# Optimization experiments

Measured on AMD Instinct MI355X. Metric: run time of the kernel, lower is better.

The kernel has to match this reference:

```python
import jax, jax.numpy as jnp
import numpy as np

LN_EPS = 1e-6  # flax.linen.LayerNorm default
ETA_BASE = 1.0  # TTTLinear default


def _ln(u, g, b):
    mu = u.mean(-1, keepdims=True)
    var = ((u - mu) ** 2).mean(-1, keepdims=True)
    return (u - mu) / jnp.sqrt(var + LN_EPS) * g + b


def setup_inputs() -> dict:
    key = jax.random.key(0)
    ks = jax.random.split(key, 8)
    B, T, D, Bd = 16, 2048, 512, 64
    s_in = 1.0 / np.sqrt(D)
    s_bn = 1.0 / np.sqrt(Bd)
    return {
        "x": jax.random.normal(ks[0], (B, T, D), jnp.float32),
        "Wk": jax.random.normal(ks[1], (D, Bd), jnp.float32) * s_in,
        "bk": jnp.zeros((Bd,), jnp.float32),
        "Wv": jax.random.normal(ks[2], (D, Bd), jnp.float32) * s_in,
        "bv": jnp.zeros((Bd,), jnp.float32),
        "Wq": jax.random.normal(ks[3], (D, Bd), jnp.float32) * s_in,
        "bq": jnp.zeros((Bd,), jnp.float32),
        "Wo": jax.random.normal(ks[4], (Bd, D), jnp.float32) * s_bn,
        "bo": jnp.zeros((D,), jnp.float32),
        "ln_g": jnp.ones((Bd,), jnp.float32),
        "ln_b": jnp.zeros((Bd,), jnp.float32),
        "lr_w": jax.random.normal(ks[5], (D,), jnp.float32) * s_in,
        "lr_b": jnp.zeros((), jnp.float32),
        "W0": jax.random.normal(ks[6], (Bd, Bd), jnp.float32) * 0.01,
    }


def reference(x, Wk, bk, Wv, bv, Wq, bq, Wo, bo, ln_g, ln_b, lr_w, lr_b, W0):
    # Sequential TTT-Linear: per-token SGD update of fast weights W (per batch element).
    B, T, D = x.shape
    Bd = W0.shape[0]

    def ssl_loss(W, k, v):
        # f(k; W) = k + LN(k @ W.T); loss = mean((f - v)^2)
        pred = k + _ln(k @ W.T, ln_g, ln_b)
        return jnp.mean((pred - v) ** 2)

    grad_fn = jax.vmap(jax.value_and_grad(ssl_loss))  # over batch

    def step(W, x_t):
        # x_t: (B, D); W: (B, Bd, Bd)
        k = x_t @ Wk + bk
        v = x_t @ Wv + bv
        loss, gW = grad_fn(W, k, v)
        eta = ETA_BASE * jax.nn.sigmoid(x_t @ lr_w + lr_b)  # (B,)
        W_new = W - eta[:, None, None] * gW
        q = x_t @ Wq + bq
        h = q + _ln(jnp.einsum('bi,boi->bo', q, W_new), ln_g, ln_b)
        z = h @ Wo + bo
        return W_new, (z, loss)

    W_init = jnp.broadcast_to(W0, (B, Bd, Bd))
    W_final, (zs, losses) = jax.lax.scan(step, W_init, jnp.swapaxes(x, 0, 1))
    z = jnp.swapaxes(zs, 0, 1)  # (B, T, D_out)
    return z
```

## Files before the change

### kernel.cpp

```cpp
#include <hip/hip_runtime.h>
#include <math.h>

#define NB 16
#define T  2048
#define D  512
#define BD 64
#define BT (NB*T)

#define OFF_K   0
#define OFF_V   (BT*BD)
#define OFF_Q   (2*BT*BD)
#define OFF_ETA (3*BT*BD)
#define OFF_H   (3*BT*BD + BT)

#define GSTRIDE 544
#define NCHUNK  (BT/16)

#define RL(x, i) __int_as_float(__builtin_amdgcn_readlane(__float_as_int(x), (i)))

__device__ __forceinline__ float wave_allsum(float x) {
  x += __int_as_float(__builtin_amdgcn_update_dpp(
      0, __float_as_int(x), 0x111, 0xf, 0xf, true));
  x += __int_as_float(__builtin_amdgcn_update_dpp(
      0, __float_as_int(x), 0x112, 0xf, 0xf, true));
  x += __int_as_float(__builtin_amdgcn_update_dpp(
      0, __float_as_int(x), 0x114, 0xf, 0xf, true));
  x += __int_as_float(__builtin_amdgcn_update_dpp(
      0, __float_as_int(x), 0x118, 0xf, 0xf, true));
  x += __int_as_float(__builtin_amdgcn_update_dpp(
      0, __float_as_int(x), 0x142, 0xa, 0xf, false));
  x += __int_as_float(__builtin_amdgcn_update_dpp(
      0, __float_as_int(x), 0x143, 0xc, 0xf, false));
  return RL(x, 63);
}

__device__ __forceinline__ void lds_barrier() {
  __builtin_amdgcn_sched_barrier(0);
  __builtin_amdgcn_s_waitcnt(0xC07F);
  __builtin_amdgcn_s_barrier();
  __builtin_amdgcn_sched_barrier(0);
}

__global__ __launch_bounds__(256) void proj_kernel(
    const float* __restrict__ x,
    const float* __restrict__ Wk, const float* __restrict__ bk,
    const float* __restrict__ Wv, const float* __restrict__ bv,
    const float* __restrict__ Wq, const float* __restrict__ bq,
    float* __restrict__ Kout, float* __restrict__ Vout,
    float* __restrict__ Qout) {
  __shared__ __align__(16) float xs[16 * D];
  const int tid = threadIdx.x;
  const size_t row0 = (size_t)blockIdx.x * 16;
  const float4* xg = (const float4*)(x + row0 * D);
  float4* xs4 = (float4*)xs;
#pragma unroll
  for (int i = 0; i < 8; i++) xs4[i * 256 + tid] = xg[i * 256 + tid];
  __syncthreads();
  const int col = tid & 63;
  const int rg = tid >> 6;

  float ak0 = 0.f, ak1 = 0.f, ak2 = 0.f, ak3 = 0.f;
  float av0 = 0.f, av1 = 0.f, av2 = 0.f, av3 = 0.f;
  float aq0 = 0.f, aq1 = 0.f, aq2 = 0.f, aq3 = 0.f;
  for (int d = 0; d < D; d += 4) {
    float wk0 = Wk[(d + 0) * BD + col];
    float wk1 = Wk[(d + 1) * BD + col];
    float wk2 = Wk[(d + 2) * BD + col];
    float wk3 = Wk[(d + 3) * BD + col];
    float wv0 = Wv[(d + 0) * BD + col];
    float wv1 = Wv[(d + 1) * BD + col];
    float wv2 = Wv[(d + 2) * BD + col];
    float wv3 = Wv[(d + 3) * BD + col];
    float wq0 = Wq[(d + 0) * BD + col];
    float wq1 = Wq[(d + 1) * BD + col];
    float wq2 = Wq[(d + 2) * BD + col];
    float wq3 = Wq[(d + 3) * BD + col];
    const float* xb = xs + (rg * 4) * D + d;
    float4 x0 = *(const float4*)(xb);
    float4 x1 = *(const float4*)(xb + D);
    float4 x2 = *(const float4*)(xb + 2 * D);
    float4 x3 = *(const float4*)(xb + 3 * D);
    ak0 += x0.x * wk0 + x0.y * wk1 + x0.z * wk2 + x0.w * wk3;
    ak1 += x1.x * wk0 + x1.y * wk1 + x1.z * wk2 + x1.w * wk3;
    ak2 += x2.x * wk0 + x2.y * wk1 + x2.z * wk2 + x2.w * wk3;
    ak3 += x3.x * wk0 + x3.y * wk1 + x3.z * wk2 + x3.w * wk3;
    av0 += x0.x * wv0 + x0.y * wv1 + x0.z * wv2 + x0.w * wv3;
    av1 += x1.x * wv0 + x1.y * wv1 + x1.z * wv2 + x1.w * wv3;
    av2 += x2.x * wv0 + x2.y * wv1 + x2.z * wv2 + x2.w * wv3;
    av3 += x3.x * wv0 + x3.y * wv1 + x3.z * wv2 + x3.w * wv3;
    aq0 += x0.x * wq0 + x0.y * wq1 + x0.z * wq2 + x0.w * wq3;
    aq1 += x1.x * wq0 + x1.y * wq1 + x1.z * wq2 + x1.w * wq3;
    aq2 += x2.x * wq0 + x2.y * wq1 + x2.z * wq2 + x2.w * wq3;
    aq3 += x3.x * wq0 + x3.y * wq1 + x3.z * wq2 + x3.w * wq3;
  }
  float bbk = bk[col], bbv = bv[col], bbq = bq[col];
  const size_t r0 = row0 + rg * 4;
  Kout[(r0 + 0) * BD + col] = ak0 + bbk;
  Kout[(r0 + 1) * BD + col] = ak1 + bbk;
  Kout[(r0 + 2) * BD + col] = ak2 + bbk;
  Kout[(r0 + 3) * BD + col] = ak3 + bbk;
  Vout[(r0 + 0) * BD + col] = av0 + bbv;
  Vout[(r0 + 1) * BD + col] = av1 + bbv;
  Vout[(r0 + 2) * BD + col] = av2 + bbv;
  Vout[(r0 + 3) * BD + col] = av3 + bbv;
  Qout[(r0 + 0) * BD + col] = aq0 + bbq;
  Qout[(r0 + 1) * BD + col] = aq1 + bbq;
  Qout[(r0 + 2) * BD + col] = aq2 + bbq;
  Qout[(r0 + 3) * BD + col] = aq3 + bbq;
}

__global__ __launch_bounds__(256) void eta_kernel(const float* __restrict__ x,
                                                  const float* __restrict__ lr_w,
                                                  const float* __restrict__ lr_b,
                                                  float* __restrict__ eta) {
  const int tid = threadIdx.x;
  const int lane = tid & 63;
  const int wv = tid >> 6;
  const size_t r = (size_t)blockIdx.x * 4 + wv;
  const float* xr = x + r * D + lane * 8;
  float4 a = *(const float4*)xr;
  float4 b = *(const float4*)(xr + 4);
  const float* lw = lr_w + lane * 8;
  float4 la = *(const float4*)lw;
  float4 lb = *(const float4*)(lw + 4);
  float p = a.x * la.x + a.y * la.y + a.z * la.z + a.w * la.w +
            b.x * lb.x + b.y * lb.y + b.z * lb.z + b.w * lb.w;
#pragma unroll
  for (int m = 32; m > 0; m >>= 1) p += __shfl_xor(p, m, 64);
  if (lane == 0) eta[r] = 1.0f / (1.0f + expf(-(p + lr_b[0])));
}

__global__ __launch_bounds__(256) void gram_kernel(
    const float* __restrict__ K, const float* __restrict__ V,
    const float* __restrict__ Q, const float* __restrict__ ln_g,
    const float* __restrict__ ln_b, float* __restrict__ G) {
  __shared__ __align__(16) float sK[16][64], sQ[16][64], sV[16][64];
  __shared__ float sg[64], sb[64];
  const int tid = threadIdx.x;
  const size_t row0 = (size_t)blockIdx.x * 16;
  ((float4*)sK)[tid] = ((const float4*)(K + row0 * BD))[tid];
  ((float4*)sQ)[tid] = ((const float4*)(Q + row0 * BD))[tid];
  ((float4*)sV)[tid] = ((const float4*)(V + row0 * BD))[tid];
  if (tid < 64) { sg[tid] = ln_g[tid]; sb[tid] = ln_b[tid]; }
  __syncthreads();
  const int i = tid >> 4, t = tid & 15;
  float kk = 0.f, kq = 0.f;
#pragma unroll
  for (int d = 0; d < 64; d += 4) {
    float4 a4 = *(const float4*)&sK[i][d];
    float4 b4 = *(const float4*)&sK[t][d];
    float4 c4 = *(const float4*)&sQ[t][d];
    kk += a4.x * b4.x + a4.y * b4.y + a4.z * b4.z + a4.w * b4.w;
    kq += a4.x * c4.x + a4.y * c4.y + a4.z * c4.z + a4.w * c4.w;
  }
  size_t gb = (size_t)blockIdx.x * GSTRIDE;
  G[gb + i * 16 + t] = kk;
  G[gb + 256 + i * 16 + t] = kq;
  if (tid < 16) {
    float sc = 0.f;
    for (int d = 0; d < 64; d++)
      sc += sg[d] * (sK[tid][d] + sb[d] - sV[tid][d]);
    G[gb + 512 + tid] = sc;
  }
}

__global__ __launch_bounds__(256, 1)
void ttt_seq_kernel(
    const float* __restrict__ Kin, const float* __restrict__ Vin,
    const float* __restrict__ Qin, const float* __restrict__ eta_in,
    const float* __restrict__ W0, const float* __restrict__ ln_g,
    const float* __restrict__ ln_b, float* __restrict__ Hout,
    const float* __restrict__ gram) {
  __shared__ __align__(16) float2 part2[16][4][64];
  __shared__ __align__(16) float kls[16][64];
  __shared__ __align__(16) float qls[16][64];
  const int tid = threadIdx.x;
  const int lane = tid & 63;
  const int wvu = __builtin_amdgcn_readfirstlane(tid) >> 6;
  const int b = blockIdx.x;

  float w[16];
  {
    const float4* w04 = (const float4*)(W0 + (size_t)lane * BD + wvu * 16);
#pragma unroll
    for (int i = 0; i < 4; i++) {
      float4 t4 = w04[i];
      w[4 * i] = t4.x; w[4 * i + 1] = t4.y; w[4 * i + 2] = t4.z; w[4 * i + 3] = t4.w;
    }
  }
  const float g = ln_g[lane];
  const float bet = ln_b[lane];
  const float a = g * g;
  const float A2 = wave_allsum(a);

  size_t base = (size_t)b * T * BD;
  size_t ebase = (size_t)b * T;

  float krow[16], qrow[16], vrow[16];
#pragma unroll
  for (int r = 0; r < 16; r++) {
    krow[r] = Kin[base + r * BD + lane];
    qrow[r] = Qin[base + r * BD + lane];
    vrow[r] = Vin[base + r * BD + lane];
  }
  float ev  = eta_in[ebase + lane];
  float evn = eta_in[ebase + 64 + lane];

  float u2sv[4], qsv[4];

  for (int c64 = 0; c64 < 32; c64++) {
    size_t eoff = (size_t)(c64 + 2) * 64;
    if (eoff >= T) eoff = 0;
    float ev2 = eta_in[ebase + eoff + lane];

    for (int cc = 0; cc < 4; cc++) {
      const size_t gb = (size_t)(b * 128 + c64 * 4 + cc) * GSTRIDE;
      float KKr[15], KQr[16];
#pragma unroll
      for (int t = 0; t < 15; t++) KKr[t] = gram[gb + t * 16 + lane];
#pragma unroll
      for (int t = 0; t < 16; t++) KQr[t] = gram[gb + 256 + t * 16 + lane];
      float SCv = gram[gb + 512 + lane];

#pragma unroll
      for (int r = 0; r < 16; r++) {
        kls[r][lane] = krow[r];
        qls[r][lane] = qrow[r];
      }
      float4 kuf[3][4], quf[3][4];
#pragma unroll
      for (int r = 0; r < 3; r++) {
        const float4* kp = (const float4*)&kls[r][wvu * 16];
        const float4* qp = (const float4*)&qls[r][wvu * 16];
#pragma unroll
        for (int i = 0; i < 4; i++) { kuf[r][i] = kp[i]; quf[r][i] = qp[i]; }
      }
      float u0[16], p0[16];
#pragma unroll
      for (int r = 0; r < 16; r++) {
        const int bf = r % 3;
        float uu0 = 0.f, uu1 = 0.f, uu2 = 0.f, uu3 = 0.f;
        float pp0 = 0.f, pp1 = 0.f, pp2 = 0.f, pp3 = 0.f;
#pragma unroll
        for (int i = 0; i < 4; i++) {
          uu0 += kuf[bf][i].x * w[4 * i + 0];
          uu1 += kuf[bf][i].y * w[4 * i + 1];
          uu2 += kuf[bf][i].z * w[4 * i + 2];
          uu3 += kuf[bf][i].w * w[4 * i + 3];
          pp0 += quf[bf][i].x * w[4 * i + 0];
          pp1 += quf[bf][i].y * w[4 * i + 1];
          pp2 += quf[bf][i].z * w[4 * i + 2];
          pp3 += quf[bf][i].w * w[4 * i + 3];
        }
        part2[r][wvu][lane] = make_float2((uu0 + uu1) + (uu2 + uu3),
                                          (pp0 + pp1) + (pp2 + pp3));
        if (r < 13) {
          const float4* kp = (const float4*)&kls[r + 3][wvu * 16];
          const float4* qp = (const float4*)&qls[r + 3][wvu * 16];
#pragma unroll
          for (int i = 0; i < 4; i++) { kuf[bf][i] = kp[i]; quf[bf][i] = qp[i]; }
        }
      }

      lds_barrier();

#pragma unroll
      for (int r = 0; r < 16; r++) {
        float2 pA = part2[r][0][lane];
        float2 pB = part2[r][1][lane];
        float2 pC = part2[r][2][lane];
        float2 pD = part2[r][3][lane];
        u0[r] = (pA.x + pB.x) + (pC.x + pD.x);
        p0[r] = (pA.y + pB.y) + (pC.y + pD.y);
      }

      float pcorr[4];
#pragma unroll
      for (int fi = 0; fi < 4; fi++) pcorr[fi] = 0.f;

#pragma unroll
      for (int t = 0; t < 16; t++) {
        float u = u0[t];
        float kcur = krow[t], vcur = vrow[t], qcur = qrow[t];
        float ecur = RL(ev, cc * 16 + t);
        float c0 = g * (kcur + bet - vcur);

        float Su   = wave_allsum(u);
        float Suu  = wave_allsum(u * u);
        float Sau  = wave_allsum(a * u);
        float Sauu = wave_allsum(a * u * u);
        float Scu  = wave_allsum(c0 * u);
        float Sc   = RL(SCv, t);

        float mu = Su * (1.0f / 64);
        float var = Suu * (1.0f / 64) - mu * mu;
        float rstd = rsqrtf(var + 1e-6f);
        float xh = (u - mu) * rstd;
        float Axh   = rstd * (Sau - mu * A2);
        float Scxh  = rstd * (Scu - mu * Sc);
        float Saxh2 = rstd * rstd * (Sauu - 2.0f * mu * Sau + mu * mu * A2);
        float s1 = (2.0f / 64) * (Sc + Axh);
        float s2 = (2.0f / 64) * (Scxh + Saxh2);
        float dxh = (2.0f / 64) * (c0 + a * xh);
        float dldu = rstd * (dxh - s1 * (1.0f / 64) - xh * (s2 * (1.0f / 64)));
        float coef = -ecur * dldu;

        if (t < 15)
          u0[t + 1] += coef * RL(KKr[t], t + 1);
#pragma unroll
        for (int s = t + 2; s < 16; s++)
          u0[s] += coef * RL(KKr[t], s);

#pragma unroll
        for (int fi = 0; fi < 4; fi++) {
          if (t <= 4 * fi + 3) {
            const int town = 4 * fi + wvu;
            float term = coef * RL(KQr[t], town);
            if (t <= town) pcorr[fi] += term;
          }
        }

        {
          const float4* kp = (const float4*)&kls[t][wvu * 16];
#pragma unroll
          for (int i = 0; i < 4; i++) {
            float4 k4 = kp[i];
            w[4 * i + 0] += coef * k4.x;
            w[4 * i + 1] += coef * k4.y;
            w[4 * i + 2] += coef * k4.z;
            w[4 * i + 3] += coef * k4.w;
          }
        }

        if ((t & 3) == wvu) { u2sv[t >> 2] = p0[t]; qsv[t >> 2] = qcur; }

        krow[t] = Kin[base + 16 * BD + lane];
        qrow[t] = Qin[base + 16 * BD + lane];
        vrow[t] = Vin[base + 16 * BD + lane];
        base += BD;
      }

#pragma unroll
      for (int fi = 0; fi < 4; fi++) {
        float u2 = u2sv[fi] + pcorr[fi];
        float Su2  = wave_allsum(u2);
        float Suu2 = wave_allsum(u2 * u2);
        float mu2 = Su2 * (1.0f / 64);
        float rstd2 = rsqrtf(Suu2 * (1.0f / 64) - mu2 * mu2 + 1e-6f);
        int tt = 4 * fi + wvu;
        Hout[base - (size_t)(16 - tt) * BD + lane] =
            qsv[fi] + (u2 - mu2) * rstd2 * g + bet;
      }

      lds_barrier();
    }
    ev = evn; evn = ev2;
  }
}

__global__ __launch_bounds__(256) void outproj_kernel(
    const float* __restrict__ H, const float* __restrict__ Wo,
    const float* __restrict__ bo, float* __restrict__ out) {
  __shared__ __align__(16) float ht[16 * BD];
  const int tid = threadIdx.x;
  const size_t row0 = (size_t)blockIdx.x * 16;
  ((float4*)ht)[tid] = ((const float4*)(H + row0 * BD))[tid];
  __syncthreads();
  float acc0[16], acc1[16];
#pragma unroll
  for (int r = 0; r < 16; r++) { acc0[r] = 0.f; acc1[r] = 0.f; }
  for (int kk = 0; kk < BD; kk++) {
    float w0 = Wo[kk * D + tid];
    float w1 = Wo[kk * D + tid + 256];
#pragma unroll
    for (int r = 0; r < 16; r++) {
      float hv = ht[r * BD + kk];
      acc0[r] += hv * w0;
      acc1[r] += hv * w1;
    }
  }
  float b0 = bo[tid], b1 = bo[tid + 256];
#pragma unroll
  for (int r = 0; r < 16; r++) {
    out[(row0 + r) * D + tid] = acc0[r] + b0;
    out[(row0 + r) * D + tid + 256] = acc1[r] + b1;
  }
}

extern "C" void kernel_launch(void* const* d_in, const int* in_sizes, int n_in,
                              void* d_out, int out_size, void* d_ws,
                              size_t ws_size, hipStream_t stream) {
  (void)in_sizes; (void)n_in; (void)out_size; (void)ws_size;
  const float* x    = (const float*)d_in[0];
  const float* Wk   = (const float*)d_in[1];
  const float* bk   = (const float*)d_in[2];
  const float* Wv   = (const float*)d_in[3];
  const float* bv   = (const float*)d_in[4];
  const float* Wq   = (const float*)d_in[5];
  const float* bq   = (const float*)d_in[6];
  const float* Wo   = (const float*)d_in[7];
  const float* bo   = (const float*)d_in[8];
  const float* ln_g = (const float*)d_in[9];
  const float* ln_b = (const float*)d_in[10];
  const float* lr_w = (const float*)d_in[11];
  const float* lr_b = (const float*)d_in[12];
  const float* W0   = (const float*)d_in[13];

  float* ws  = (float*)d_ws;
  float* Kb  = ws + OFF_K;
  float* Vb  = ws + OFF_V;
  float* Qb  = ws + OFF_Q;
  float* ETA = ws + OFF_ETA;
  float* Hb  = ws + OFF_H;
  float* out = (float*)d_out;
  float* GRAM = out;

  proj_kernel<<<BT / 16, 256, 0, stream>>>(x, Wk, bk, Wv, bv, Wq, bq, Kb, Vb, Qb);
  eta_kernel<<<BT / 4, 256, 0, stream>>>(x, lr_w, lr_b, ETA);
  gram_kernel<<<NCHUNK, 256, 0, stream>>>(Kb, Vb, Qb, ln_g, ln_b, GRAM);
  ttt_seq_kernel<<<NB, 256, 0, stream>>>(Kb, Vb, Qb, ETA, W0, ln_g, ln_b, Hb, GRAM);
  outproj_kernel<<<BT / 16, 256, 0, stream>>>(Hb, Wo, bo, out);
}
```

Baseline: 1.621 ms.

## Fuse eta and gram into projection kernel, restructure KQ correction and outproj

Folds the eta (sigmoid learning-rate) computation and the per-chunk Gram matrix computation into the projection kernel, reusing x and K/Q/V already in shared memory. This removes two launches and the global reloads of x, K, Q and V. In the sequential kernel, the KQ correction is now added directly into p0 for every later row instead of into a separate per-wave pcorr array, which adds more readlane work per step. The output projection loop is also unrolled by four with float4 reads of H.

```diff
diff --git a/kernel.cpp b/kernel.cpp
--- a/kernel.cpp
+++ b/kernel.cpp
@@ -46,18 +46,25 @@
     const float* __restrict__ Wk, const float* __restrict__ bk,
     const float* __restrict__ Wv, const float* __restrict__ bv,
     const float* __restrict__ Wq, const float* __restrict__ bq,
+    const float* __restrict__ lr_w, const float* __restrict__ lr_b,
+    const float* __restrict__ ln_g, const float* __restrict__ ln_b,
     float* __restrict__ Kout, float* __restrict__ Vout,
-    float* __restrict__ Qout) {
+    float* __restrict__ Qout, float* __restrict__ eta,
+    float* __restrict__ G) {
   __shared__ __align__(16) float xs[16 * D];
+  __shared__ __align__(16) float sK[16][64], sQ[16][64], sV[16][64];
+  __shared__ float sg[64], sb[64];
   const int tid = threadIdx.x;
   const size_t row0 = (size_t)blockIdx.x * 16;
   const float4* xg = (const float4*)(x + row0 * D);
   float4* xs4 = (float4*)xs;
 #pragma unroll
   for (int i = 0; i < 8; i++) xs4[i * 256 + tid] = xg[i * 256 + tid];
+  if (tid < 64) { sg[tid] = ln_g[tid]; sb[tid] = ln_b[tid]; }
   __syncthreads();
   const int col = tid & 63;
   const int rg = tid >> 6;
+  const int lane = tid & 63;
 
   float ak0 = 0.f, ak1 = 0.f, ak2 = 0.f, ak3 = 0.f;
   float av0 = 0.f, av1 = 0.f, av2 = 0.f, av3 = 0.f;
@@ -95,67 +102,61 @@
   }
   float bbk = bk[col], bbv = bv[col], bbq = bq[col];
   const size_t r0 = row0 + rg * 4;
-  Kout[(r0 + 0) * BD + col] = ak0 + bbk;
-  Kout[(r0 + 1) * BD + col] = ak1 + bbk;
-  Kout[(r0 + 2) * BD + col] = ak2 + bbk;
-  Kout[(r0 + 3) * BD + col] = ak3 + bbk;
-  Vout[(r0 + 0) * BD + col] = av0 + bbv;
-  Vout[(r0 + 1) * BD + col] = av1 + bbv;
-  Vout[(r0 + 2) * BD + col] = av2 + bbv;
-  Vout[(r0 + 3) * BD + col] = av3 + bbv;
-  Qout[(r0 + 0) * BD + col] = aq0 + bbq;
-  Qout[(r0 + 1) * BD + col] = aq1 + bbq;
-  Qout[(r0 + 2) * BD + col] = aq2 + bbq;
-  Qout[(r0 + 3) * BD + col] = aq3 + bbq;
-}
-
-__global__ __launch_bounds__(256) void eta_kernel(const float* __restrict__ x,
-                                                  const float* __restrict__ lr_w,
-                                                  const float* __restrict__ lr_b,
-                                                  float* __restrict__ eta) {
-  const int tid = threadIdx.x;
-  const int lane = tid & 63;
-  const int wv = tid >> 6;
-  const size_t r = (size_t)blockIdx.x * 4 + wv;
-  const float* xr = x + r * D + lane * 8;
-  float4 a = *(const float4*)xr;
-  float4 b = *(const float4*)(xr + 4);
-  const float* lw = lr_w + lane * 8;
-  float4 la = *(const float4*)lw;
-  float4 lb = *(const float4*)(lw + 4);
-  float p = a.x * la.x + a.y * la.y + a.z * la.z + a.w * la.w +
-            b.x * lb.x + b.y * lb.y + b.z * lb.z + b.w * lb.w;
-#pragma unroll
-  for (int m = 32; m > 0; m >>= 1) p += __shfl_xor(p, m, 64);
-  if (lane == 0) eta[r] = 1.0f / (1.0f + expf(-(p + lr_b[0])));
-}
-
-__global__ __launch_bounds__(256) void gram_kernel(
-    const float* __restrict__ K, const float* __restrict__ V,
-    const float* __restrict__ Q, const float* __restrict__ ln_g,
-    const float* __restrict__ ln_b, float* __restrict__ G) {
-  __shared__ __align__(16) float sK[16][64], sQ[16][64], sV[16][64];
-  __shared__ float sg[64], sb[64];
-  const int tid = threadIdx.x;
-  const size_t row0 = (size_t)blockIdx.x * 16;
-  ((float4*)sK)[tid] = ((const float4*)(K + row0 * BD))[tid];
-  ((float4*)sQ)[tid] = ((const float4*)(Q + row0 * BD))[tid];
-  ((float4*)sV)[tid] = ((const float4*)(V + row0 * BD))[tid];
-  if (tid < 64) { sg[tid] = ln_g[tid]; sb[tid] = ln_b[tid]; }
+  float k0v = ak0 + bbk, k1v = ak1 + bbk, k2v = ak2 + bbk, k3v = ak3 + bbk;
+  float v0v = av0 + bbv, v1v = av1 + bbv, v2v = av2 + bbv, v3v = av3 + bbv;
+  float q0v = aq0 + bbq, q1v = aq1 + bbq, q2v = aq2 + bbq, q3v = aq3 + bbq;
+  Kout[(r0 + 0) * BD + col] = k0v;
+  Kout[(r0 + 1) * BD + col] = k1v;
+  Kout[(r0 + 2) * BD + col] = k2v;
+  Kout[(r0 + 3) * BD + col] = k3v;
+  Vout[(r0 + 0) * BD + col] = v0v;
+  Vout[(r0 + 1) * BD + col] = v1v;
+  Vout[(r0 + 2) * BD + col] = v2v;
+  Vout[(r0 + 3) * BD + col] = v3v;
+  Qout[(r0 + 0) * BD + col] = q0v;
+  Qout[(r0 + 1) * BD + col] = q1v;
+  Qout[(r0 + 2) * BD + col] = q2v;
+  Qout[(r0 + 3) * BD + col] = q3v;
+  const int lr = rg * 4;
+  sK[lr + 0][col] = k0v; sK[lr + 1][col] = k1v;
+  sK[lr + 2][col] = k2v; sK[lr + 3][col] = k3v;
+  sV[lr + 0][col] = v0v; sV[lr + 1][col] = v1v;
+  sV[lr + 2][col] = v2v; sV[lr + 3][col] = v3v;
+  sQ[lr + 0][col] = q0v; sQ[lr + 1][col] = q1v;
+  sQ[lr + 2][col] = q2v; sQ[lr + 3][col] = q3v;
+
+  {
+    const float* lw = lr_w + lane * 8;
+    float4 la = *(const float4*)lw;
+    float4 lb = *(const float4*)(lw + 4);
+    float lrb0 = lr_b[0];
+#pragma unroll
+    for (int j = 0; j < 4; j++) {
+      const float* xr = xs + (size_t)(rg * 4 + j) * D + lane * 8;
+      float4 a = *(const float4*)xr;
+      float4 b2 = *(const float4*)(xr + 4);
+      float p = a.x * la.x + a.y * la.y + a.z * la.z + a.w * la.w +
+                b2.x * lb.x + b2.y * lb.y + b2.z * lb.z + b2.w * lb.w;
+#pragma unroll
+      for (int m = 32; m > 0; m >>= 1) p += __shfl_xor(p, m, 64);
+      if (lane == 0) eta[row0 + rg * 4 + j] = 1.0f / (1.0f + expf(-(p + lrb0)));
+    }
+  }
   __syncthreads();
-  const int i = tid >> 4, t = tid & 15;
+
+  const int gi = tid >> 4, gt = tid & 15;
   float kk = 0.f, kq = 0.f;
 #pragma unroll
   for (int d = 0; d < 64; d += 4) {
-    float4 a4 = *(const float4*)&sK[i][d];
-    float4 b4 = *(const float4*)&sK[t][d];
-    float4 c4 = *(const float4*)&sQ[t][d];
+    float4 a4 = *(const float4*)&sK[gi][d];
+    float4 b4 = *(const float4*)&sK[gt][d];
+    float4 c4 = *(const float4*)&sQ[gt][d];
     kk += a4.x * b4.x + a4.y * b4.y + a4.z * b4.z + a4.w * b4.w;
     kq += a4.x * c4.x + a4.y * c4.y + a4.z * c4.z + a4.w * c4.w;
   }
   size_t gb = (size_t)blockIdx.x * GSTRIDE;
-  G[gb + i * 16 + t] = kk;
-  G[gb + 256 + i * 16 + t] = kq;
+  G[gb + gi * 16 + gt] = kk;
+  G[gb + 256 + gi * 16 + gt] = kq;
   if (tid < 16) {
     float sc = 0.f;
     for (int d = 0; d < 64; d++)
@@ -274,10 +275,6 @@
         p0[r] = (pA.y + pB.y) + (pC.y + pD.y);
       }
 
-      float pcorr[4];
-#pragma unroll
-      for (int fi = 0; fi < 4; fi++) pcorr[fi] = 0.f;
-
 #pragma unroll
       for (int t = 0; t < 16; t++) {
         float u = u0[t];
@@ -310,15 +307,9 @@
 #pragma unroll
         for (int s = t + 2; s < 16; s++)
           u0[s] += coef * RL(KKr[t], s);
-
-#pragma unroll
-        for (int fi = 0; fi < 4; fi++) {
-          if (t <= 4 * fi + 3) {
-            const int town = 4 * fi + wvu;
-            float term = coef * RL(KQr[t], town);
-            if (t <= town) pcorr[fi] += term;
-          }
-        }
+#pragma unroll
+        for (int s = t; s < 16; s++)
+          p0[s] += coef * RL(KQr[t], s);
 
         {
           const float4* kp = (const float4*)&kls[t][wvu * 16];
@@ -342,7 +333,7 @@
 
 #pragma unroll
       for (int fi = 0; fi < 4; fi++) {
-        float u2 = u2sv[fi] + pcorr[fi];
+        float u2 = u2sv[fi];
         float Su2  = wave_allsum(u2);
         float Suu2 = wave_allsum(u2 * u2);
         float mu2 = Su2 * (1.0f / 64);
@@ -369,14 +360,26 @@
   float acc0[16], acc1[16];
 #pragma unroll
   for (int r = 0; r < 16; r++) { acc0[r] = 0.f; acc1[r] = 0.f; }
-  for (int kk = 0; kk < BD; kk++) {
-    float w0 = Wo[kk * D + tid];
-    float w1 = Wo[kk * D + tid + 256];
+  for (int kk4 = 0; kk4 < 16; kk4++) {
+    float w00 = Wo[(4 * kk4 + 0) * D + tid];
+    float w01 = Wo[(4 * kk4 + 1) * D + tid];
+    float w02 = Wo[(4 * kk4 + 2) * D + tid];
+    float w03 = Wo[(4 * kk4 + 3) * D + tid];
+    float w10 = Wo[(4 * kk4 + 0) * D + tid + 256];
+    float w11 = Wo[(4 * kk4 + 1) * D + tid + 256];
+    float w12 = Wo[(4 * kk4 + 2) * D + tid + 256];
+    float w13 = Wo[(4 * kk4 + 3) * D + tid + 256];
 #pragma unroll
     for (int r = 0; r < 16; r++) {
-      float hv = ht[r * BD + kk];
-      acc0[r] += hv * w0;
-      acc1[r] += hv * w1;
+      float4 hv = *(const float4*)&ht[r * BD + 4 * kk4];
+      acc0[r] += hv.x * w00;
+      acc0[r] += hv.y * w01;
+      acc0[r] += hv.z * w02;
+      acc0[r] += hv.w * w03;
+      acc1[r] += hv.x * w10;
+      acc1[r] += hv.y * w11;
+      acc1[r] += hv.z * w12;
+      acc1[r] += hv.w * w13;
     }
   }
   float b0 = bo[tid], b1 = bo[tid + 256];
@@ -415,9 +418,9 @@
   float* out = (float*)d_out;
   float* GRAM = out;
 
-  proj_kernel<<<BT / 16, 256, 0, stream>>>(x, Wk, bk, Wv, bv, Wq, bq, Kb, Vb, Qb);
-  eta_kernel<<<BT / 4, 256, 0, stream>>>(x, lr_w, lr_b, ETA);
-  gram_kernel<<<NCHUNK, 256, 0, stream>>>(Kb, Vb, Qb, ln_g, ln_b, GRAM);
+  proj_kernel<<<NCHUNK, 256, 0, stream>>>(x, Wk, bk, Wv, bv, Wq, bq,
+                                          lr_w, lr_b, ln_g, ln_b,
+                                          Kb, Vb, Qb, ETA, GRAM);
   ttt_seq_kernel<<<NB, 256, 0, stream>>>(Kb, Vb, Qb, ETA, W0, ln_g, ln_b, Hb, GRAM);
   outproj_kernel<<<BT / 16, 256, 0, stream>>>(Hb, Wo, bo, out);
 }
```

Result: faster. 1.403 ms (-13.5%).
